# Kernel optimization log

Hardware: AMD Instinct MI355X
Metric: run time of the kernel (lower is better)

Reference implementation:

```python
import jax, jax.numpy as jnp
import numpy as np

INF = 1e6  # stands in for +infinity in the distance transform (fp32-safe when squared)


def _edt(sites):
    """Exact Euclidean distance to the nearest True pixel.
    sites: bool [N, H, W] -> float32 [N, H, W].
    Pass 1: exact 1D distance along width via min-plus cumulative scans.
    Pass 2: lower envelope over rows, d2[y] = min_y' (g[y']^2 + (y-y')^2),
    computed row-by-row with lax.map to avoid an [N,H,W,H] intermediate.
    """
    N, H, W = sites.shape
    pen = jnp.where(sites, 0.0, INF).astype(jnp.float32)  # 0 at sites, INF elsewhere
    xs = jnp.arange(W, dtype=jnp.float32)
    # d_fwd[i] = min_{j<=i} (i - j + pen[j]);  d_bwd[i] = min_{j>=i} (j - i + pen[j])
    fwd = xs + jax.lax.cummin(pen - xs, axis=2)
    bwd = -xs + jax.lax.cummin(pen + xs, axis=2, reverse=True)
    g = jnp.minimum(fwd, bwd)  # exact 1D distance along width
    g2 = g * g
    ys = jnp.arange(H, dtype=jnp.float32)

    def row_min(y):
        # min over source row y' of g2[:, y', :] + (y - y')^2  -> [N, W]
        return jnp.min(g2 + ((y - ys) ** 2)[None, :, None], axis=1)

    d2 = jax.lax.map(row_min, ys)  # [H, N, W]
    return jnp.sqrt(jnp.transpose(d2, (1, 0, 2)))


def _phi(mask):
    """Signed level-set function: -dist_inside on foreground, +dist_outside on background.
    mask: bool [B, H, W]. Images with empty foreground get all-zero phi (as in the torch code).
    """
    sites = jnp.concatenate([~mask, mask], axis=0)  # nearest-background / nearest-foreground
    d = _edt(sites)
    B = mask.shape[0]
    din, dout = d[:B], d[B:]
    phi = jnp.where(mask, -din, dout)
    phi = jnp.where(jnp.abs(phi) > 1e5, 0.0, phi)  # guard degenerate (no-site) cases
    any_fg = jnp.any(mask, axis=(1, 2))
    return jnp.where(any_fg[:, None, None], phi, 0.0)


def setup_inputs() -> dict:
    key = jax.random.key(0)
    k1, k2 = jax.random.split(key)
    predictions = jax.random.normal(k1, (16, 1, 512, 512), dtype=jnp.float32)
    targets = jax.random.randint(k2, (16, 1, 512, 512), 0, 2, dtype=jnp.int32)
    return {"predictions": predictions, "targets": targets}


def reference(predictions, targets):
    alpha = 0.01      # initial_alpha, 'rebalance' schedule at epoch 0
    smooth = 1e-6
    p = jax.nn.sigmoid(predictions)
    t = targets.astype(jnp.float32)
    # Dice loss
    inter = jnp.sum(p * t)
    dice = 1.0 - (2.0 * inter + smooth) / (jnp.sum(p) + jnp.sum(t) + smooth)
    # Boundary loss
    phi = _phi(targets[:, 0].astype(bool))[:, None]  # [B,1,H,W]
    boundary = jnp.mean(phi * p)
    return (1.0 - alpha) * dice + alpha * boundary
```

## Files before the change

kernel.cpp:

```cpp
#include <hip/hip_runtime.h>


#define NPIX (16 * 512 * 512)
#define NB2  4096
#define SENT 65535.0f

__global__ __launch_bounds__(256) void edt_rows_both(const int* __restrict__ t,
                                                     unsigned short* __restrict__ g,
                                                     unsigned char* __restrict__ mb) {
    const int wave = threadIdx.x >> 6;
    const int lane = threadIdx.x & 63;
    const int row  = (blockIdx.x << 2) + wave;
    const int base = row << 9;
    const int x0   = lane << 3;

    const int4* tp = (const int4*)(t + base + x0);
    int4 ta = tp[0], tb = tp[1];
    int tv[8] = {ta.x, ta.y, ta.z, ta.w, tb.x, tb.y, tb.z, tb.w};

    float pen[2][8];
    unsigned int mybyte = 0;
#pragma unroll
    for (int i = 0; i < 8; ++i) {
        bool fg = (tv[i] != 0);
        pen[0][i] = fg ? 1.0e6f : 0.0f;
        pen[1][i] = fg ? 0.0f : 1.0e6f;
        mybyte |= (fg ? 1u : 0u) << i;
    }
    mb[(row << 6) + lane] = (unsigned char)mybyte;

    const float BIG = 3.0e37f;

#pragma unroll
    for (int f = 0; f < 2; ++f) {
        float pf[8];
        float run = BIG;
#pragma unroll
        for (int i = 0; i < 8; ++i) { run = fminf(run, pen[f][i] - (float)(x0 + i)); pf[i] = run; }
        float incl = run;
#pragma unroll
        for (int off = 1; off < 64; off <<= 1) {
            float u = __shfl_up(incl, (unsigned)off, 64);
            if (lane >= off) incl = fminf(incl, u);
        }
        float excl = __shfl_up(incl, 1u, 64);
        if (lane == 0) excl = BIG;

        float sf[8];
        run = BIG;
#pragma unroll
        for (int i = 7; i >= 0; --i) { run = fminf(run, pen[f][i] + (float)(x0 + i)); sf[i] = run; }
        float inclb = run;
#pragma unroll
        for (int off = 1; off < 64; off <<= 1) {
            float u = __shfl_down(inclb, (unsigned)off, 64);
            if (lane + off < 64) inclb = fminf(inclb, u);
        }
        float exclb = __shfl_down(inclb, 1u, 64);
        if (lane == 63) exclb = BIG;

        unsigned int pk[4];
#pragma unroll
        for (int i = 0; i < 8; i += 2) {
            float xa = (float)(x0 + i);
            float fa = xa + fminf(pf[i], excl);
            float ba = -xa + fminf(sf[i], exclb);
            float ga = fminf(fminf(fa, ba), SENT);
            float xb = (float)(x0 + i + 1);
            float fb = xb + fminf(pf[i + 1], excl);
            float bb = -xb + fminf(sf[i + 1], exclb);
            float gb = fminf(fminf(fb, bb), SENT);
            pk[i >> 1] = (unsigned int)ga | ((unsigned int)gb << 16);
        }
        uint4 outv = {pk[0], pk[1], pk[2], pk[3]};
        *((uint4*)(g + (size_t)f * NPIX + base + x0)) = outv;
    }
}

__global__ __launch_bounds__(256) void edt_cols_loss(const float* __restrict__ pred,
                                                     const unsigned short* __restrict__ g,
                                                     const unsigned int* __restrict__ mw,
                                                     double* __restrict__ partials) {
    const int tid  = blockIdx.x * 256 + threadIdx.x;
    const int idx0 = tid << 2;
    const int n    = idx0 >> 18;
    const int y    = (idx0 >> 9) & 511;
    const int x    = idx0 & 511;

    const unsigned int bits = (mw[idx0 >> 5] >> (idx0 & 31)) & 0xF;

    const float4 p4 = *((const float4*)(pred + idx0));
    float pv[4] = {p4.x, p4.y, p4.z, p4.w};

    const ushort4 g0v = *((const ushort4*)(g + idx0));
    const ushort4 g1v = *((const ushort4*)(g + NPIX + idx0));
    const unsigned short g0a[4] = {g0v.x, g0v.y, g0v.z, g0v.w};
    const unsigned short g1a[4] = {g1v.x, g1v.y, g1v.z, g1v.w};

    const unsigned short* gcv[4];
    float m2[4];
    float mx = 0.0f;
#pragma unroll
    for (int j = 0; j < 4; ++j) {
        bool fg = (bits >> j) & 1;
        float gv = (float)(fg ? g0a[j] : g1a[j]);
        m2[j] = gv * gv;
        mx = fmaxf(mx, m2[j]);
        gcv[j] = g + (fg ? 0 : NPIX) + (n << 18) + x + j;
    }

    for (int k = 1; k < 512; ++k) {
        float k2 = (float)(k * k);
        if (k2 >= mx) break;
        int yd = y - k;
        int yu = y + k;
        mx = 0.0f;
#pragma unroll
        for (int j = 0; j < 4; ++j) {
            if (k2 < m2[j]) {
                if (yd >= 0) {
                    float gg = (float)gcv[j][yd << 9];
                    m2[j] = fminf(m2[j], fmaf(gg, gg, k2));
                }
                if (yu < 512) {
                    float gg = (float)gcv[j][yu << 9];
                    m2[j] = fminf(m2[j], fmaf(gg, gg, k2));
                }
            }
            mx = fmaxf(mx, m2[j]);
        }
    }

    double s_b = 0.0, s_p = 0.0, s_i = 0.0;
    int s_t = 0;
#pragma unroll
    for (int j = 0; j < 4; ++j) {
        bool fg = (bits >> j) & 1;
        float p = 1.0f / (1.0f + expf(-pv[j]));
        float d = sqrtf(m2[j]);
        float phi = fg ? -d : d;
        if (d > 1.0e4f) phi = 0.0f;
        s_b += (double)(phi * p);
        s_p += (double)p;
        if (fg) { s_i += (double)p; s_t += 1; }
    }
    double s_tt = (double)s_t;

#pragma unroll
    for (int off = 32; off > 0; off >>= 1) {
        s_b  += __shfl_xor(s_b,  off, 64);
        s_p  += __shfl_xor(s_p,  off, 64);
        s_i  += __shfl_xor(s_i,  off, 64);
        s_tt += __shfl_xor(s_tt, off, 64);
    }
    __shared__ double sred[4][4];
    const int wave = threadIdx.x >> 6;
    const int lane = threadIdx.x & 63;
    if (lane == 0) {
        sred[wave][0] = s_b; sred[wave][1] = s_p; sred[wave][2] = s_i; sred[wave][3] = s_tt;
    }
    __syncthreads();
    if (threadIdx.x == 0) {
        double* dst = partials + (size_t)blockIdx.x * 4;
#pragma unroll
        for (int c = 0; c < 4; ++c)
            dst[c] = sred[0][c] + sred[1][c] + sred[2][c] + sred[3][c];
    }
}

__global__ __launch_bounds__(256) void finalize_loss(const double* __restrict__ partials,
                                                     float* __restrict__ out) {
    __shared__ double red[256][4];
    double s0 = 0.0, s1 = 0.0, s2 = 0.0, s3 = 0.0;
    for (int i = threadIdx.x; i < NB2; i += 256) {
        const double* src = partials + (size_t)i * 4;
        s0 += src[0]; s1 += src[1]; s2 += src[2]; s3 += src[3];
    }
    red[threadIdx.x][0] = s0;
    red[threadIdx.x][1] = s1;
    red[threadIdx.x][2] = s2;
    red[threadIdx.x][3] = s3;
    __syncthreads();
    for (int s = 128; s > 0; s >>= 1) {
        if (threadIdx.x < s) {
            red[threadIdx.x][0] += red[threadIdx.x + s][0];
            red[threadIdx.x][1] += red[threadIdx.x + s][1];
            red[threadIdx.x][2] += red[threadIdx.x + s][2];
            red[threadIdx.x][3] += red[threadIdx.x + s][3];
        }
        __syncthreads();
    }
    if (threadIdx.x == 0) {
        double sb = red[0][0];
        double sp = red[0][1];
        double si = red[0][2];
        double st = red[0][3];
        double dice = 1.0 - (2.0 * si + 1e-6) / (sp + st + 1e-6);
        double boundary = sb / (double)NPIX;
        out[0] = (float)(0.99 * dice + 0.01 * boundary);
    }
}

extern "C" void kernel_launch(void* const* d_in, const int* in_sizes, int n_in,
                              void* d_out, int out_size, void* d_ws, size_t ws_size,
                              hipStream_t stream) {
    const float* pred = (const float*)d_in[0];
    const int*   targ = (const int*)d_in[1];
    unsigned short* gfield = (unsigned short*)d_ws;
    unsigned char*  mbytes = (unsigned char*)d_ws + (size_t)NPIX * 4;
    double* partials = (double*)((char*)d_ws + (size_t)NPIX * 4 + NPIX / 8);
    float* out = (float*)d_out;

    edt_rows_both<<<2048, 256, 0, stream>>>(targ, gfield, mbytes);
    edt_cols_loss<<<NB2, 256, 0, stream>>>(pred, gfield, (const unsigned int*)mbytes, partials);
    finalize_loss<<<1, 256, 0, stream>>>(partials, out);
}
```

Before: 98.93 us.

## Fuse row and column EDT passes into one LDS-tiled kernel with halo and fallback

```diff
diff --git a/kernel.cpp b/kernel.cpp
--- a/kernel.cpp
+++ b/kernel.cpp
@@ -1,148 +1,187 @@
 #include <hip/hip_runtime.h>
 
 
-#define NPIX (16 * 512 * 512)
-#define NB2  4096
+#define HH 512
+#define WW 512
+#define BH 32
+#define HALO 16
+#define TR 64
+#define NT 512
+#define NBLK 256
 #define SENT 65535.0f
 
-__global__ __launch_bounds__(256) void edt_rows_both(const int* __restrict__ t,
-                                                     unsigned short* __restrict__ g,
-                                                     unsigned char* __restrict__ mb) {
-    const int wave = threadIdx.x >> 6;
-    const int lane = threadIdx.x & 63;
-    const int row  = (blockIdx.x << 2) + wave;
-    const int base = row << 9;
-    const int x0   = lane << 3;
-
-    const int4* tp = (const int4*)(t + base + x0);
-    int4 ta = tp[0], tb = tp[1];
-    int tv[8] = {ta.x, ta.y, ta.z, ta.w, tb.x, tb.y, tb.z, tb.w};
-
-    float pen[2][8];
-    unsigned int mybyte = 0;
-#pragma unroll
-    for (int i = 0; i < 8; ++i) {
-        bool fg = (tv[i] != 0);
-        pen[0][i] = fg ? 1.0e6f : 0.0f;
-        pen[1][i] = fg ? 0.0f : 1.0e6f;
-        mybyte |= (fg ? 1u : 0u) << i;
-    }
-    mb[(row << 6) + lane] = (unsigned char)mybyte;
-
+__device__ float fallback_exact(const int* __restrict__ t, int n, int y, int x,
+                                bool fg, float m2) {
+    const int* tn = t + (n << 18);
+    for (int yy = 0; yy < HH; ++yy) {
+        float dy = (float)(yy - y);
+        float dy2 = dy * dy;
+        if (dy2 >= m2) continue;
+        const int* row = tn + (yy << 9);
+        int lim = (int)sqrtf(m2 - dy2);
+        for (int dx = 0; dx <= lim; ++dx) {
+            bool hit = false;
+            int xl = x - dx, xr = x + dx;
+            if (xl >= 0) { int v = row[xl]; hit = fg ? (v == 0) : (v != 0); }
+            if (!hit && xr < WW) { int v = row[xr]; hit = fg ? (v == 0) : (v != 0); }
+            if (hit) {
+                float c = fmaf((float)dx, (float)dx, dy2);
+                if (c < m2) m2 = c;
+                break;
+            }
+        }
+    }
+    return m2;
+}
+
+__global__ __launch_bounds__(NT, 1) void edt_fused(const int* __restrict__ t,
+                                                   const float* __restrict__ pred,
+                                                   double* __restrict__ partials) {
+    __shared__ unsigned int gl[TR][WW];
+    __shared__ double sred[8][4];
+
+    const int n     = blockIdx.x >> 4;
+    const int y0    = (blockIdx.x & 15) << 5;
+    const int rbase = y0 - HALO;
+    const int wave  = threadIdx.x >> 6;
+    const int lane  = threadIdx.x & 63;
+    const int x0    = lane << 3;
     const float BIG = 3.0e37f;
 
-#pragma unroll
-    for (int f = 0; f < 2; ++f) {
-        float pf[8];
-        float run = BIG;
-#pragma unroll
-        for (int i = 0; i < 8; ++i) { run = fminf(run, pen[f][i] - (float)(x0 + i)); pf[i] = run; }
-        float incl = run;
-#pragma unroll
-        for (int off = 1; off < 64; off <<= 1) {
-            float u = __shfl_up(incl, (unsigned)off, 64);
-            if (lane >= off) incl = fminf(incl, u);
-        }
-        float excl = __shfl_up(incl, 1u, 64);
-        if (lane == 0) excl = BIG;
-
-        float sf[8];
-        run = BIG;
-#pragma unroll
-        for (int i = 7; i >= 0; --i) { run = fminf(run, pen[f][i] + (float)(x0 + i)); sf[i] = run; }
-        float inclb = run;
-#pragma unroll
-        for (int off = 1; off < 64; off <<= 1) {
-            float u = __shfl_down(inclb, (unsigned)off, 64);
-            if (lane + off < 64) inclb = fminf(inclb, u);
-        }
-        float exclb = __shfl_down(inclb, 1u, 64);
-        if (lane == 63) exclb = BIG;
-
-        unsigned int pk[4];
-#pragma unroll
-        for (int i = 0; i < 8; i += 2) {
-            float xa = (float)(x0 + i);
-            float fa = xa + fminf(pf[i], excl);
-            float ba = -xa + fminf(sf[i], exclb);
-            float ga = fminf(fminf(fa, ba), SENT);
-            float xb = (float)(x0 + i + 1);
-            float fb = xb + fminf(pf[i + 1], excl);
-            float bb = -xb + fminf(sf[i + 1], exclb);
-            float gb = fminf(fminf(fb, bb), SENT);
-            pk[i >> 1] = (unsigned int)ga | ((unsigned int)gb << 16);
-        }
-        uint4 outv = {pk[0], pk[1], pk[2], pk[3]};
-        *((uint4*)(g + (size_t)f * NPIX + base + x0)) = outv;
-    }
-}
-
-__global__ __launch_bounds__(256) void edt_cols_loss(const float* __restrict__ pred,
-                                                     const unsigned short* __restrict__ g,
-                                                     const unsigned int* __restrict__ mw,
-                                                     double* __restrict__ partials) {
-    const int tid  = blockIdx.x * 256 + threadIdx.x;
-    const int idx0 = tid << 2;
-    const int n    = idx0 >> 18;
-    const int y    = (idx0 >> 9) & 511;
-    const int x    = idx0 & 511;
-
-    const unsigned int bits = (mw[idx0 >> 5] >> (idx0 & 31)) & 0xF;
-
-    const float4 p4 = *((const float4*)(pred + idx0));
-    float pv[4] = {p4.x, p4.y, p4.z, p4.w};
-
-    const ushort4 g0v = *((const ushort4*)(g + idx0));
-    const ushort4 g1v = *((const ushort4*)(g + NPIX + idx0));
-    const unsigned short g0a[4] = {g0v.x, g0v.y, g0v.z, g0v.w};
-    const unsigned short g1a[4] = {g1v.x, g1v.y, g1v.z, g1v.w};
-
-    const unsigned short* gcv[4];
-    float m2[4];
-    float mx = 0.0f;
-#pragma unroll
-    for (int j = 0; j < 4; ++j) {
-        bool fg = (bits >> j) & 1;
-        float gv = (float)(fg ? g0a[j] : g1a[j]);
-        m2[j] = gv * gv;
-        mx = fmaxf(mx, m2[j]);
-        gcv[j] = g + (fg ? 0 : NPIX) + (n << 18) + x + j;
-    }
-
-    for (int k = 1; k < 512; ++k) {
-        float k2 = (float)(k * k);
-        if (k2 >= mx) break;
-        int yd = y - k;
-        int yu = y + k;
-        mx = 0.0f;
-#pragma unroll
-        for (int j = 0; j < 4; ++j) {
-            if (k2 < m2[j]) {
-                if (yd >= 0) {
-                    float gg = (float)gcv[j][yd << 9];
-                    m2[j] = fminf(m2[j], fmaf(gg, gg, k2));
-                }
-                if (yu < 512) {
-                    float gg = (float)gcv[j][yu << 9];
-                    m2[j] = fminf(m2[j], fmaf(gg, gg, k2));
-                }
-            }
-            mx = fmaxf(mx, m2[j]);
-        }
-    }
+    for (int rr = wave; rr < TR; rr += 8) {
+        const int gy = rbase + rr;
+        if (gy < 0 || gy >= HH) {
+            uint4 s = {0xFFFFFFFFu, 0xFFFFFFFFu, 0xFFFFFFFFu, 0xFFFFFFFFu};
+            *((uint4*)&gl[rr][x0])     = s;
+            *((uint4*)&gl[rr][x0 + 4]) = s;
+            continue;
+        }
+        const int4* tp = (const int4*)(t + (n << 18) + (gy << 9) + x0);
+        int4 ta = tp[0], tb = tp[1];
+        int tv[8] = {ta.x, ta.y, ta.z, ta.w, tb.x, tb.y, tb.z, tb.w};
+
+        float pen[2][8];
+#pragma unroll
+        for (int i = 0; i < 8; ++i) {
+            bool fg = (tv[i] != 0);
+            pen[0][i] = fg ? 1.0e6f : 0.0f;
+            pen[1][i] = fg ? 0.0f : 1.0e6f;
+        }
+
+        unsigned short gout[2][8];
+#pragma unroll
+        for (int f = 0; f < 2; ++f) {
+            float pf[8];
+            float run = BIG;
+#pragma unroll
+            for (int i = 0; i < 8; ++i) { run = fminf(run, pen[f][i] - (float)(x0 + i)); pf[i] = run; }
+            float incl = run;
+#pragma unroll
+            for (int off = 1; off < 64; off <<= 1) {
+                float u = __shfl_up(incl, (unsigned)off, 64);
+                if (lane >= off) incl = fminf(incl, u);
+            }
+            float excl = __shfl_up(incl, 1u, 64);
+            if (lane == 0) excl = BIG;
+
+            float sf[8];
+            run = BIG;
+#pragma unroll
+            for (int i = 7; i >= 0; --i) { run = fminf(run, pen[f][i] + (float)(x0 + i)); sf[i] = run; }
+            float inclb = run;
+#pragma unroll
+            for (int off = 1; off < 64; off <<= 1) {
+                float u = __shfl_down(inclb, (unsigned)off, 64);
+                if (lane + off < 64) inclb = fminf(inclb, u);
+            }
+            float exclb = __shfl_down(inclb, 1u, 64);
+            if (lane == 63) exclb = BIG;
+
+#pragma unroll
+            for (int i = 0; i < 8; ++i) {
+                float xa = (float)(x0 + i);
+                float fa = xa + fminf(pf[i], excl);
+                float ba = -xa + fminf(sf[i], exclb);
+                gout[f][i] = (unsigned short)fminf(fminf(fa, ba), SENT);
+            }
+        }
+
+        unsigned int pk[8];
+#pragma unroll
+        for (int i = 0; i < 8; ++i)
+            pk[i] = (unsigned int)gout[0][i] | ((unsigned int)gout[1][i] << 16);
+        uint4 o0 = {pk[0], pk[1], pk[2], pk[3]};
+        uint4 o1 = {pk[4], pk[5], pk[6], pk[7]};
+        *((uint4*)&gl[rr][x0])     = o0;
+        *((uint4*)&gl[rr][x0 + 4]) = o1;
+    }
+    __syncthreads();
 
     double s_b = 0.0, s_p = 0.0, s_i = 0.0;
     int s_t = 0;
-#pragma unroll
-    for (int j = 0; j < 4; ++j) {
-        bool fg = (bits >> j) & 1;
-        float p = 1.0f / (1.0f + expf(-pv[j]));
-        float d = sqrtf(m2[j]);
-        float phi = fg ? -d : d;
-        if (d > 1.0e4f) phi = 0.0f;
-        s_b += (double)(phi * p);
-        s_p += (double)p;
-        if (fg) { s_i += (double)p; s_t += 1; }
+
+#pragma unroll 1
+    for (int grp = 0; grp < 8; ++grp) {
+        const int pid = (grp * NT + threadIdx.x) << 2;
+        const int yl  = pid >> 9;
+        const int x   = pid & 511;
+        const int r   = yl + HALO;
+
+        const float4 p4 = *((const float4*)(pred + (n << 18) + ((y0 + yl) << 9) + x));
+        const float pv[4] = {p4.x, p4.y, p4.z, p4.w};
+
+        const uint4 ow = *((const uint4*)&gl[r][x]);
+        const unsigned int w[4] = {ow.x, ow.y, ow.z, ow.w};
+
+        bool  fg[4];
+        float m2[4];
+        float mx = 0.0f;
+#pragma unroll
+        for (int j = 0; j < 4; ++j) {
+            unsigned int lo = w[j] & 0xFFFFu, hi = w[j] >> 16;
+            fg[j] = (hi == 0u);
+            float gv = (float)(fg[j] ? lo : hi);
+            m2[j] = gv * gv;
+            mx = fmaxf(mx, m2[j]);
+        }
+
+        for (int k = 1; k <= HALO; ++k) {
+            float k2 = (float)(k * k);
+            if (k2 >= mx) break;
+            const uint4 wd4 = *((const uint4*)&gl[r - k][x]);
+            const uint4 wu4 = *((const uint4*)&gl[r + k][x]);
+            const unsigned int wd[4] = {wd4.x, wd4.y, wd4.z, wd4.w};
+            const unsigned int wu[4] = {wu4.x, wu4.y, wu4.z, wu4.w};
+            mx = 0.0f;
+#pragma unroll
+            for (int j = 0; j < 4; ++j) {
+                if (k2 < m2[j]) {
+                    unsigned int a = fg[j] ? (wd[j] & 0xFFFFu) : (wd[j] >> 16);
+                    unsigned int b = fg[j] ? (wu[j] & 0xFFFFu) : (wu[j] >> 16);
+                    float fa = (float)a, fb = (float)b;
+                    m2[j] = fminf(m2[j], fminf(fmaf(fa, fa, k2), fmaf(fb, fb, k2)));
+                }
+                mx = fmaxf(mx, m2[j]);
+            }
+        }
+
+        if (mx > 289.0f) {
+#pragma unroll
+            for (int j = 0; j < 4; ++j)
+                if (m2[j] > 289.0f)
+                    m2[j] = fallback_exact(t, n, y0 + yl, x + j, fg[j], m2[j]);
+        }
+
+#pragma unroll
+        for (int j = 0; j < 4; ++j) {
+            float p = 1.0f / (1.0f + expf(-pv[j]));
+            float d = sqrtf(m2[j]);
+            float phi = fg[j] ? -d : d;
+            if (d > 1.0e4f) phi = 0.0f;
+            s_b += (double)(phi * p);
+            s_p += (double)p;
+            if (fg[j]) { s_i += (double)p; s_t += 1; }
+        }
     }
     double s_tt = (double)s_t;
 
@@ -153,9 +192,6 @@
         s_i  += __shfl_xor(s_i,  off, 64);
         s_tt += __shfl_xor(s_tt, off, 64);
     }
-    __shared__ double sred[4][4];
-    const int wave = threadIdx.x >> 6;
-    const int lane = threadIdx.x & 63;
     if (lane == 0) {
         sred[wave][0] = s_b; sred[wave][1] = s_p; sred[wave][2] = s_i; sred[wave][3] = s_tt;
     }
@@ -163,40 +199,38 @@
     if (threadIdx.x == 0) {
         double* dst = partials + (size_t)blockIdx.x * 4;
 #pragma unroll
-        for (int c = 0; c < 4; ++c)
-            dst[c] = sred[0][c] + sred[1][c] + sred[2][c] + sred[3][c];
+        for (int c = 0; c < 4; ++c) {
+            double acc = 0.0;
+#pragma unroll
+            for (int wv = 0; wv < 8; ++wv) acc += sred[wv][c];
+            dst[c] = acc;
+        }
     }
 }
 
 __global__ __launch_bounds__(256) void finalize_loss(const double* __restrict__ partials,
                                                      float* __restrict__ out) {
-    __shared__ double red[256][4];
-    double s0 = 0.0, s1 = 0.0, s2 = 0.0, s3 = 0.0;
-    for (int i = threadIdx.x; i < NB2; i += 256) {
-        const double* src = partials + (size_t)i * 4;
-        s0 += src[0]; s1 += src[1]; s2 += src[2]; s3 += src[3];
-    }
-    red[threadIdx.x][0] = s0;
-    red[threadIdx.x][1] = s1;
-    red[threadIdx.x][2] = s2;
-    red[threadIdx.x][3] = s3;
+    const int wave = threadIdx.x >> 6;
+    const int lane = threadIdx.x & 63;
+    const double* src = partials + (size_t)threadIdx.x * 4;
+    double s0 = src[0], s1 = src[1], s2 = src[2], s3 = src[3];
+#pragma unroll
+    for (int off = 32; off > 0; off >>= 1) {
+        s0 += __shfl_xor(s0, off, 64);
+        s1 += __shfl_xor(s1, off, 64);
+        s2 += __shfl_xor(s2, off, 64);
+        s3 += __shfl_xor(s3, off, 64);
+    }
+    __shared__ double red[4][4];
+    if (lane == 0) { red[wave][0] = s0; red[wave][1] = s1; red[wave][2] = s2; red[wave][3] = s3; }
     __syncthreads();
-    for (int s = 128; s > 0; s >>= 1) {
-        if (threadIdx.x < s) {
-            red[threadIdx.x][0] += red[threadIdx.x + s][0];
-            red[threadIdx.x][1] += red[threadIdx.x + s][1];
-            red[threadIdx.x][2] += red[threadIdx.x + s][2];
-            red[threadIdx.x][3] += red[threadIdx.x + s][3];
-        }
-        __syncthreads();
-    }
     if (threadIdx.x == 0) {
-        double sb = red[0][0];
-        double sp = red[0][1];
-        double si = red[0][2];
-        double st = red[0][3];
+        double sb = red[0][0] + red[1][0] + red[2][0] + red[3][0];
+        double sp = red[0][1] + red[1][1] + red[2][1] + red[3][1];
+        double si = red[0][2] + red[1][2] + red[2][2] + red[3][2];
+        double st = red[0][3] + red[1][3] + red[2][3] + red[3][3];
         double dice = 1.0 - (2.0 * si + 1e-6) / (sp + st + 1e-6);
-        double boundary = sb / (double)NPIX;
+        double boundary = sb / (double)(16 * 512 * 512);
         out[0] = (float)(0.99 * dice + 0.01 * boundary);
     }
 }
@@ -206,12 +240,9 @@
                               hipStream_t stream) {
     const float* pred = (const float*)d_in[0];
     const int*   targ = (const int*)d_in[1];
-    unsigned short* gfield = (unsigned short*)d_ws;
-    unsigned char*  mbytes = (unsigned char*)d_ws + (size_t)NPIX * 4;
-    double* partials = (double*)((char*)d_ws + (size_t)NPIX * 4 + NPIX / 8);
+    double* partials = (double*)d_ws;
     float* out = (float*)d_out;
 
-    edt_rows_both<<<2048, 256, 0, stream>>>(targ, gfield, mbytes);
-    edt_cols_loss<<<NB2, 256, 0, stream>>>(pred, gfield, (const unsigned int*)mbytes, partials);
+    edt_fused<<<NBLK, NT, 0, stream>>>(targ, pred, partials);
     finalize_loss<<<1, 256, 0, stream>>>(partials, out);
 }
```

Result: faster. 94.83 us (-4.1%).
